# Kernel tuning notes

Measured on AMD Instinct MI355X. Metric: run time of the kernel, lower is better.

The kernel has to match this reference:

```python
import jax, jax.numpy as jnp
import numpy as np

B, T, D_IN, H, E = 256, 512, 256, 256, 96  # batch, enc seq, input_size, hidden_size, num_embeddings


def setup_inputs() -> dict:
    key = jax.random.key(0)
    ks = jax.random.split(key, 12)
    s = 0.05
    return {
        "prev_h": jax.random.normal(ks[0], (B, H), jnp.float32),
        "prev_c": jax.random.normal(ks[1], (B, H), jnp.float32),
        "batch_H": jax.random.normal(ks[2], (B, T, D_IN), jnp.float32),
        "char_onehots": jax.random.uniform(ks[3], (B, E), jnp.float32),
        "W_i2h": jax.random.normal(ks[4], (H, D_IN), jnp.float32) * s,
        "W_h2h": jax.random.normal(ks[5], (H, H), jnp.float32) * s,
        "b_h2h": jax.random.normal(ks[6], (H,), jnp.float32) * s,
        "W_score": jax.random.normal(ks[7], (1, H), jnp.float32) * s,
        "W_ih": jax.random.normal(ks[8], (4 * H, D_IN + E), jnp.float32) * s,
        "W_hh": jax.random.normal(ks[9], (4 * H, H), jnp.float32) * s,
        "b_ih": jax.random.normal(ks[10], (4 * H,), jnp.float32) * s,
        "b_hh": jax.random.normal(ks[11], (4 * H,), jnp.float32) * s,
    }


def reference(prev_h, prev_c, batch_H, char_onehots,
              W_i2h, W_h2h, b_h2h, W_score, W_ih, W_hh, b_ih, b_hh):
    # additive attention over encoder features
    proj = jnp.einsum('btd,hd->bth', batch_H, W_i2h)          # [B,T,H]
    hid = prev_h @ W_h2h.T + b_h2h                             # [B,H]
    e = jnp.einsum('bth,oh->bto', jnp.tanh(proj + hid[:, None, :]), W_score)  # [B,T,1]
    alpha = jax.nn.softmax(e, axis=1)                          # [B,T,1]
    context = jnp.einsum('bt,btd->bd', alpha[..., 0], batch_H) # [B,D_IN]
    x = jnp.concatenate([context, char_onehots], axis=1)       # [B,D_IN+E]
    # LSTM cell step (PyTorch gate order: i, f, g, o)
    gates = x @ W_ih.T + b_ih + prev_h @ W_hh.T + b_hh         # [B,4H]
    i, f, g, o = jnp.split(gates, 4, axis=1)
    c_new = jax.nn.sigmoid(f) * prev_c + jax.nn.sigmoid(i) * jnp.tanh(g)
    h_new = jax.nn.sigmoid(o) * jnp.tanh(c_new)
    return (h_new, c_new, jnp.swapaxes(alpha, 1, 2))           # alpha -> [B,1,T]
```

## Files before the change

### kernel.cpp

```cpp
#include <hip/hip_runtime.h>

typedef __attribute__((ext_vector_type(8))) short short8;
typedef __attribute__((ext_vector_type(4))) float f32x4;

#define KPAD 40
#define APITCH 264

#define WS_HID   0u
#define WS_P     262144u
#define WS_Z     786432u
#define WS_CTX   794624u
#define WS_CTXP  1056768u
#define WS_WBF   3153920u

__device__ __forceinline__ unsigned cvtpk(float lo, float hi) {
    unsigned r;
    asm("v_cvt_pk_bf16_f32 %0, %1, %2" : "=v"(r) : "v"(lo), "v"(hi));
    return r;
}
__device__ __forceinline__ int4 pack8(float4 x0, float4 x1) {
    int4 q;
    q.x = (int)cvtpk(x0.x, x0.y);
    q.y = (int)cvtpk(x0.z, x0.w);
    q.z = (int)cvtpk(x1.x, x1.y);
    q.w = (int)cvtpk(x1.z, x1.w);
    return q;
}
__device__ __forceinline__ float bf2f(unsigned s) {
    union { float f; unsigned u; } v; v.u = s << 16;
    return v.f;
}
__device__ __forceinline__ float tanh_fast(float x) {
    float e2 = __expf(2.f * x);
    return 1.f - 2.f * __builtin_amdgcn_rcpf(e2 + 1.f);
}
__device__ __forceinline__ float sigmoid_fast(float x) {
    return __builtin_amdgcn_rcpf(1.f + __expf(-x));
}
__device__ __forceinline__ void gload16(const void* g, void* l) {
    __builtin_amdgcn_global_load_lds((const __attribute__((address_space(1))) void*)g,
                                     (__attribute__((address_space(3))) void*)l, 16, 0, 0);
}

__global__ __launch_bounds__(256) void k_prep(
    const float* __restrict__ prev_h, const float* __restrict__ W_i2h,
    const float* __restrict__ W_h2h, const float* __restrict__ b_h2h,
    float* __restrict__ hid, short* __restrict__ Wbf)
{
    int bid = blockIdx.x, tid = threadIdx.x;
    if (bid < 256) {
        __shared__ float ph[256];
        ph[tid] = prev_h[bid * 256 + tid];
        __syncthreads();
        float acc = b_h2h[tid];
        const float4* w = (const float4*)(W_h2h + tid * 256);
        #pragma unroll 8
        for (int k4 = 0; k4 < 64; ++k4) {
            float4 ww = w[k4];
            acc += ww.x * ph[k4*4+0] + ww.y * ph[k4*4+1] + ww.z * ph[k4*4+2] + ww.w * ph[k4*4+3];
        }
        hid[bid * 256 + tid] = acc;
    } else {
        int idx = (bid - 256) * 256 + tid;
        int kc = idx / (256 * KPAD);
        int rem = idx % (256 * KPAD);
        int n = rem / KPAD, kk = rem % KPAD;
        float v = 0.f;
        if (kk < 32) {
            union { float f; unsigned u; } t; t.f = W_i2h[n * 256 + kc * 32 + kk];
            t.u = (t.u + 0x7FFFu + ((t.u >> 16) & 1u)) & 0xFFFF0000u;
            v = t.f;
        }
        union { float f; unsigned u; } o; o.f = v;
        Wbf[idx] = (short)(o.u >> 16);
    }
}

__global__ __launch_bounds__(256, 2) void k_escore_ctx(
    const float* __restrict__ BH, const short* __restrict__ Wbf,
    const float* __restrict__ hid, const float* __restrict__ Wsc,
    float* __restrict__ p_out, float* __restrict__ zbuf, float* __restrict__ ctxp)
{
    __shared__ char smem[74752];
    short* Al = (short*)smem;
    char*  BlB = smem + 33792;
    short* Bl = (short*)BlB;
    float* eps = (float*)BlB;
    float* pl  = (float*)(BlB + 1024);
    float* r4  = (float*)(BlB + 1280);

    const int tid = threadIdx.x;
    const int lane = tid & 63;
    const int w = tid >> 6;
    const int l15 = lane & 15, lg = lane >> 4;
    const int bt0 = blockIdx.x * 64;
    const int b = bt0 >> 9;
    const int c = (bt0 >> 6) & 7;

    {
        const char* gs0 = (const char*)Wbf + tid * 16;
        #pragma unroll
        for (int s = 0; s < 5; ++s)
            gload16(gs0 + s * 4096, BlB + s * 4096 + tid * 16);
    }
    {
        const float* as = BH + (size_t)bt0 * 256 + tid * 8;
        const int row0 = tid >> 5, colw = (tid & 31) * 8;
        #pragma unroll
        for (int i = 0; i < 8; ++i) {
            float4 x0 = *(const float4*)(as + i * 2048);
            float4 x1 = *(const float4*)(as + i * 2048 + 4);
            *(int4*)&Al[(i * 8 + row0) * APITCH + colw] = pack8(x0, x1);
        }
    }
    __syncthreads();

    f32x4 acc[4][4];
    #pragma unroll
    for (int i = 0; i < 4; i++)
        #pragma unroll
        for (int j = 0; j < 4; j++) acc[i][j] = (f32x4){0.f, 0.f, 0.f, 0.f};

    #pragma unroll
    for (int ks = 0; ks < 8; ++ks) {
        const int cur = ks & 1;
        if (ks < 7) {
            const char* gsb = (const char*)Wbf + (size_t)(ks + 1) * 20480 + tid * 16;
            char* lsb = BlB + (cur ^ 1) * 20480 + tid * 16;
            #pragma unroll
            for (int s = 0; s < 5; ++s)
                gload16(gsb + s * 4096, lsb + s * 4096);
        }
        short8 af[4], bfr[4];
        #pragma unroll
        for (int rf = 0; rf < 4; rf++)
            af[rf] = *(const short8*)&Al[(rf * 16 + l15) * APITCH + ks * 32 + lg * 8];
        #pragma unroll
        for (int cf = 0; cf < 4; cf++)
            bfr[cf] = *(const short8*)&Bl[cur * 10240 + (w * 64 + cf * 16 + l15) * KPAD + lg * 8];
        #pragma unroll
        for (int rf = 0; rf < 4; rf++)
            #pragma unroll
            for (int cf = 0; cf < 4; cf++)
                acc[rf][cf] = __builtin_amdgcn_mfma_f32_16x16x32_bf16(af[rf], bfr[cf], acc[rf][cf], 0, 0, 0);
        __syncthreads();
    }

    float esum[4][4];
    #pragma unroll
    for (int rf = 0; rf < 4; rf++)
        #pragma unroll
        for (int r = 0; r < 4; r++) esum[rf][r] = 0.f;

    #pragma unroll
    for (int cf = 0; cf < 4; cf++) {
        int col = w * 64 + cf * 16 + l15;
        float wsv = Wsc[col];
        float hd = hid[b * 256 + col];
        #pragma unroll
        for (int rf = 0; rf < 4; rf++)
            #pragma unroll
            for (int r = 0; r < 4; r++)
                esum[rf][r] += wsv * tanh_fast(acc[rf][cf][r] + hd);
    }
    #pragma unroll
    for (int rf = 0; rf < 4; rf++)
        #pragma unroll
        for (int r = 0; r < 4; r++) {
            float s = esum[rf][r];
            s += __shfl_xor(s, 1); s += __shfl_xor(s, 2);
            s += __shfl_xor(s, 4); s += __shfl_xor(s, 8);
            esum[rf][r] = s;
        }
    if (l15 == 0) {
        #pragma unroll
        for (int rf = 0; rf < 4; rf++)
            #pragma unroll
            for (int r = 0; r < 4; r++)
                eps[w * 64 + rf * 16 + lg * 4 + r] = esum[rf][r];
    }
    __syncthreads();

    if (tid < 64) {
        float e = eps[tid] + eps[64 + tid] + eps[128 + tid] + eps[192 + tid];
        float p = __expf(e);
        p_out[bt0 + tid] = p;
        pl[tid] = p;
        float z = p;
        z += __shfl_xor(z, 1); z += __shfl_xor(z, 2); z += __shfl_xor(z, 4);
        z += __shfl_xor(z, 8); z += __shfl_xor(z, 16); z += __shfl_xor(z, 32);
        if (tid == 0) zbuf[blockIdx.x] = z;
    }
    __syncthreads();

    {
        float c0 = 0.f, c1 = 0.f, c2 = 0.f, c3 = 0.f;
        #pragma unroll
        for (int t = 0; t < 16; ++t) {
            int row = w * 16 + t;
            float pv = pl[row];
            unsigned v1 = *(const unsigned*)&Al[row * APITCH + lane * 2];
            unsigned v2 = *(const unsigned*)&Al[row * APITCH + 128 + lane * 2];
            c0 += pv * bf2f(v1 & 0xffffu); c1 += pv * bf2f(v1 >> 16);
            c2 += pv * bf2f(v2 & 0xffffu); c3 += pv * bf2f(v2 >> 16);
        }
        r4[w * 256 + lane * 2]       = c0;
        r4[w * 256 + lane * 2 + 1]   = c1;
        r4[w * 256 + 128 + lane * 2] = c2;
        r4[w * 256 + 129 + lane * 2] = c3;
    }
    __syncthreads();
    ctxp[((size_t)(c * 256 + b)) * 256 + tid] = r4[tid] + r4[256 + tid] + r4[512 + tid] + r4[768 + tid];
}

__global__ __launch_bounds__(256) void k_finalize(
    const float* __restrict__ p, const float* __restrict__ zbuf,
    const float* __restrict__ ctxp, float* __restrict__ alpha, float* __restrict__ ctx)
{
    int b = blockIdx.x, t = threadIdx.x;
    float Z = 0.f;
    #pragma unroll
    for (int cc = 0; cc < 8; ++cc) Z += zbuf[b * 8 + cc];
    float inv = 1.f / Z;
    alpha[b * 512 + t] = p[b * 512 + t] * inv;
    alpha[b * 512 + 256 + t] = p[b * 512 + 256 + t] * inv;
    float s = 0.f;
    #pragma unroll
    for (int cc = 0; cc < 8; ++cc) s += ctxp[((size_t)(cc * 256 + b)) * 256 + t];
    ctx[b * 256 + t] = s * inv;
}

__global__ __launch_bounds__(256) void k_gates_lstm(
    const float* __restrict__ ctx, const float* __restrict__ onehot,
    const float* __restrict__ prev_h, const float* __restrict__ W_ih,
    const float* __restrict__ W_hh, const float* __restrict__ b_ih,
    const float* __restrict__ b_hh, const float* __restrict__ prev_c,
    float* __restrict__ out)
{
    __shared__ char smem[20800];
    short* AlB = (short*)smem;
    short* BlB = (short*)smem + 5120;
    const int tid = threadIdx.x;
    const int lane = tid & 63;
    const int w = tid >> 6;
    const int l15 = lane & 15, lg = lane >> 4;
    const int rb = blockIdx.x * 64;
    const int hb = blockIdx.y;

    f32x4 acc[4];
    #pragma unroll
    for (int j = 0; j < 4; j++) acc[j] = (f32x4){0.f, 0.f, 0.f, 0.f};

    const int arow = tid >> 2, akg = tid & 3;
    const int rg = rb + arow;
    const int bn = tid >> 2, bq = tid & 3;
    const int np_ = hb * 64 + bn, hh_ = np_ >> 2, gg_ = np_ & 3;
    const float* wih_row = W_ih + (size_t)(gg_ * 256 + hh_) * 352;
    const float* whh_row = W_hh + (size_t)(gg_ * 256 + hh_) * 256;

    auto stageAB = [&](int kc, int bu) {
        int k0 = kc * 32 + akg * 8;
        const float4* pa;
        if (k0 < 256)      pa = (const float4*)(ctx    + rg * 256 + k0);
        else if (k0 < 352) pa = (const float4*)(onehot + rg * 96  + (k0 - 256));
        else               pa = (const float4*)(prev_h + rg * 256 + (k0 - 352));
        float4 x0 = pa[0], x1 = pa[1];
        *(int4*)&AlB[bu * 2560 + arow * KPAD + akg * 8] = pack8(x0, x1);
        int kb = kc * 32 + bq * 8;
        const float* pb = (kb < 352) ? (wih_row + kb) : (whh_row + (kb - 352));
        float4 y0 = *(const float4*)pb, y1 = *(const float4*)(pb + 4);
        *(int4*)&BlB[bu * 2560 + bn * KPAD + bq * 8] = pack8(y0, y1);
    };

    stageAB(0, 0);
    __syncthreads();

    for (int kc = 0; kc < 19; ++kc) {
        int cur = kc & 1;
        short8 af = *(const short8*)&AlB[cur * 2560 + (w * 16 + l15) * KPAD + lg * 8];
        short8 bfr[4];
        #pragma unroll
        for (int cf = 0; cf < 4; cf++)
            bfr[cf] = *(const short8*)&BlB[cur * 2560 + (cf * 16 + l15) * KPAD + lg * 8];
        if (kc < 18) stageAB(kc + 1, cur ^ 1);
        #pragma unroll
        for (int cf = 0; cf < 4; cf++)
            acc[cf] = __builtin_amdgcn_mfma_f32_16x16x32_bf16(af, bfr[cf], acc[cf], 0, 0, 0);
        __syncthreads();
    }

    float* Gt = (float*)smem;
    #pragma unroll
    for (int cf = 0; cf < 4; cf++) {
        int col = cf * 16 + l15;
        int np = hb * 64 + col;
        int hg = np >> 2, g = np & 3;
        float bias = b_ih[g * 256 + hg] + b_hh[g * 256 + hg];
        #pragma unroll
        for (int r = 0; r < 4; r++)
            Gt[(w * 16 + lg * 4 + r) * 65 + col] = acc[cf][r] + bias;
    }
    __syncthreads();

    #pragma unroll
    for (int it = 0; it < 4; ++it) {
        int elem = it * 256 + tid;
        int row = elem >> 4, hl = elem & 15;
        float gi = Gt[row * 65 + hl * 4 + 0];
        float gf = Gt[row * 65 + hl * 4 + 1];
        float gg = Gt[row * 65 + hl * 4 + 2];
        float go = Gt[row * 65 + hl * 4 + 3];
        int bg = rb + row, hglob = hb * 16 + hl;
        float cv = sigmoid_fast(gf) * prev_c[bg * 256 + hglob] + sigmoid_fast(gi) * tanh_fast(gg);
        out[bg * 256 + hglob] = sigmoid_fast(go) * tanh_fast(cv);
        out[65536 + bg * 256 + hglob] = cv;
    }
}

extern "C" void kernel_launch(void* const* d_in, const int* in_sizes, int n_in,
                              void* d_out, int out_size, void* d_ws, size_t ws_size,
                              hipStream_t stream) {
    (void)in_sizes; (void)n_in; (void)out_size; (void)ws_size;
    const float* prev_h  = (const float*)d_in[0];
    const float* prev_c  = (const float*)d_in[1];
    const float* batch_H = (const float*)d_in[2];
    const float* onehot  = (const float*)d_in[3];
    const float* W_i2h   = (const float*)d_in[4];
    const float* W_h2h   = (const float*)d_in[5];
    const float* b_h2h   = (const float*)d_in[6];
    const float* W_score = (const float*)d_in[7];
    const float* W_ih    = (const float*)d_in[8];
    const float* W_hh    = (const float*)d_in[9];
    const float* b_ih    = (const float*)d_in[10];
    const float* b_hh    = (const float*)d_in[11];

    char* ws = (char*)d_ws;
    float* hid   = (float*)(ws + WS_HID);
    float* p     = (float*)(ws + WS_P);
    float* zbuf  = (float*)(ws + WS_Z);
    float* ctx   = (float*)(ws + WS_CTX);
    float* ctxp  = (float*)(ws + WS_CTXP);
    short* Wbf   = (short*)(ws + WS_WBF);

    float* out = (float*)d_out;
    float* alpha = out + 131072;

    hipLaunchKernelGGL(k_prep,       dim3(576),    dim3(256), 0, stream,
                       prev_h, W_i2h, W_h2h, b_h2h, hid, Wbf);
    hipLaunchKernelGGL(k_escore_ctx, dim3(2048),   dim3(256), 0, stream,
                       batch_H, Wbf, hid, W_score, p, zbuf, ctxp);
    hipLaunchKernelGGL(k_finalize,   dim3(256),    dim3(256), 0, stream,
                       p, zbuf, ctxp, alpha, ctx);
    hipLaunchKernelGGL(k_gates_lstm, dim3(4, 16),  dim3(256), 0, stream,
                       ctx, onehot, prev_h, W_ih, W_hh, b_ih, b_hh, prev_c, out);
}
```

Measured before the change: 73.62 us.

## Hold W_i2h bf16 fragments in registers instead of double-buffered LDS

The weight matrix is now stored as plain row-major bf16. Each wave loads its whole B-operand slice (4x8 short8 fragments, 128 VGPRs) straight from global memory into registers up front. This removes the per-k-step global-to-LDS double buffering, the B-fragment LDS reads and the per-step __syncthreads, and shrinks shared memory. The prep kernel also converts eight floats per thread with packed bf16 conversion, so it launches half as many blocks. The large register footprint plus the existing 16 accumulators may lower occupancy or cause spills under launch_bounds(256,2).

```diff
diff --git a/kernel.cpp b/kernel.cpp
--- a/kernel.cpp
+++ b/kernel.cpp
@@ -36,10 +36,6 @@
 }
 __device__ __forceinline__ float sigmoid_fast(float x) {
     return __builtin_amdgcn_rcpf(1.f + __expf(-x));
-}
-__device__ __forceinline__ void gload16(const void* g, void* l) {
-    __builtin_amdgcn_global_load_lds((const __attribute__((address_space(1))) void*)g,
-                                     (__attribute__((address_space(3))) void*)l, 16, 0, 0);
 }
 
 __global__ __launch_bounds__(256) void k_prep(
@@ -61,18 +57,10 @@
         }
         hid[bid * 256 + tid] = acc;
     } else {
-        int idx = (bid - 256) * 256 + tid;
-        int kc = idx / (256 * KPAD);
-        int rem = idx % (256 * KPAD);
-        int n = rem / KPAD, kk = rem % KPAD;
-        float v = 0.f;
-        if (kk < 32) {
-            union { float f; unsigned u; } t; t.f = W_i2h[n * 256 + kc * 32 + kk];
-            t.u = (t.u + 0x7FFFu + ((t.u >> 16) & 1u)) & 0xFFFF0000u;
-            v = t.f;
-        }
-        union { float f; unsigned u; } o; o.f = v;
-        Wbf[idx] = (short)(o.u >> 16);
+        int idx = ((bid - 256) * 256 + tid) * 8;
+        float4 x0 = *(const float4*)(W_i2h + idx);
+        float4 x1 = *(const float4*)(W_i2h + idx + 4);
+        *(int4*)&Wbf[idx] = pack8(x0, x1);
     }
 }
 
@@ -81,13 +69,10 @@
     const float* __restrict__ hid, const float* __restrict__ Wsc,
     float* __restrict__ p_out, float* __restrict__ zbuf, float* __restrict__ ctxp)
 {
-    __shared__ char smem[74752];
-    short* Al = (short*)smem;
-    char*  BlB = smem + 33792;
-    short* Bl = (short*)BlB;
-    float* eps = (float*)BlB;
-    float* pl  = (float*)(BlB + 1024);
-    float* r4  = (float*)(BlB + 1280);
+    __shared__ short Al[64 * APITCH];
+    __shared__ float eps[4 * 64];
+    __shared__ float pl[64];
+    __shared__ float r4[4 * 256];
 
     const int tid = threadIdx.x;
     const int lane = tid & 63;
@@ -95,14 +80,18 @@
     const int l15 = lane & 15, lg = lane >> 4;
     const int bt0 = blockIdx.x * 64;
     const int b = bt0 >> 9;
-    const int c = (bt0 >> 6) & 7;
-
+    const int c = blockIdx.x & 7;
+
+    short8 breg[4][8];
     {
-        const char* gs0 = (const char*)Wbf + tid * 16;
-        #pragma unroll
-        for (int s = 0; s < 5; ++s)
-            gload16(gs0 + s * 4096, BlB + s * 4096 + tid * 16);
-    }
+        const short* bb = Wbf + (size_t)(w * 64 + l15) * 256 + lg * 8;
+        #pragma unroll
+        for (int cf = 0; cf < 4; cf++)
+            #pragma unroll
+            for (int ks = 0; ks < 8; ks++)
+                breg[cf][ks] = *(const short8*)(bb + (size_t)cf * 16 * 256 + ks * 32);
+    }
+
     {
         const float* as = BH + (size_t)bt0 * 256 + tid * 8;
         const int row0 = tid >> 5, colw = (tid & 31) * 8;
@@ -123,27 +112,15 @@
 
     #pragma unroll
     for (int ks = 0; ks < 8; ++ks) {
-        const int cur = ks & 1;
-        if (ks < 7) {
-            const char* gsb = (const char*)Wbf + (size_t)(ks + 1) * 20480 + tid * 16;
-            char* lsb = BlB + (cur ^ 1) * 20480 + tid * 16;
-            #pragma unroll
-            for (int s = 0; s < 5; ++s)
-                gload16(gsb + s * 4096, lsb + s * 4096);
-        }
-        short8 af[4], bfr[4];
+        short8 af[4];
         #pragma unroll
         for (int rf = 0; rf < 4; rf++)
             af[rf] = *(const short8*)&Al[(rf * 16 + l15) * APITCH + ks * 32 + lg * 8];
-        #pragma unroll
-        for (int cf = 0; cf < 4; cf++)
-            bfr[cf] = *(const short8*)&Bl[cur * 10240 + (w * 64 + cf * 16 + l15) * KPAD + lg * 8];
         #pragma unroll
         for (int rf = 0; rf < 4; rf++)
             #pragma unroll
             for (int cf = 0; cf < 4; cf++)
-                acc[rf][cf] = __builtin_amdgcn_mfma_f32_16x16x32_bf16(af[rf], bfr[cf], acc[rf][cf], 0, 0, 0);
-        __syncthreads();
+                acc[rf][cf] = __builtin_amdgcn_mfma_f32_16x16x32_bf16(af[rf], breg[cf][ks], acc[rf][cf], 0, 0, 0);
     }
 
     float esum[4][4];
@@ -345,7 +322,7 @@
     float* out = (float*)d_out;
     float* alpha = out + 131072;
 
-    hipLaunchKernelGGL(k_prep,       dim3(576),    dim3(256), 0, stream,
+    hipLaunchKernelGGL(k_prep,       dim3(288),    dim3(256), 0, stream,
                        prev_h, W_i2h, W_h2h, b_h2h, hid, Wbf);
     hipLaunchKernelGGL(k_escore_ctx, dim3(2048),   dim3(256), 0, stream,
                        batch_H, Wbf, hid, W_score, p, zbuf, ctxp);
```

After: 78.59 us. +6.8%, slower.
